# Kernel optimization log

Measured on AMD Instinct MI355X. Metric: run time of the kernel, lower is better.

The kernel has to match this reference:

```python
import jax, jax.numpy as jnp
import numpy as np

N_NODES = 100000
N_EDGES = 600000
IN_CH = 64
HID = 256


def setup_inputs() -> dict:
    key = jax.random.key(0)
    ks = jax.random.split(key, 8)
    x = jax.random.normal(ks[0], (N_NODES, IN_CH), dtype=jnp.float32)
    edge_index = jax.random.randint(ks[1], (2, N_EDGES), 0, N_NODES, dtype=jnp.int64)
    # Glorot-ish init for weights, zero bias (matches PyG GCNConv defaults)
    W1 = jax.random.normal(ks[2], (IN_CH, HID), dtype=jnp.float32) * (1.0 / np.sqrt(IN_CH))
    b1 = jnp.zeros((HID,), dtype=jnp.float32)
    W2 = jax.random.normal(ks[3], (HID, HID), dtype=jnp.float32) * (1.0 / np.sqrt(HID))
    b2 = jnp.zeros((HID,), dtype=jnp.float32)
    W3 = jax.random.normal(ks[4], (HID, HID), dtype=jnp.float32) * (1.0 / np.sqrt(HID))
    b3 = jnp.zeros((HID,), dtype=jnp.float32)
    return {"x": x, "edge_index": edge_index, "W1": W1, "b1": b1,
            "W2": W2, "b2": b2, "W3": W3, "b3": b3}


def _gcn_conv(x, src, dst, norm, W, b):
    # PyG GCNConv (add_self_loops=False): h = x W; out_i = sum_{j->i} norm_ij h_j; out += b
    h = x @ W                                   # [N, d_out]
    msg = h[src] * norm[:, None]                # [E, d_out] gather + scale
    out = jax.ops.segment_sum(msg, dst, num_segments=x.shape[0])
    return out + b


def reference(x, edge_index, W1, b1, W2, b2, W3, b3):
    src, dst = edge_index[0], edge_index[1]
    # symmetric degree normalization (gcn_norm without self loops)
    deg = jax.ops.segment_sum(jnp.ones_like(dst, dtype=x.dtype), dst,
                              num_segments=x.shape[0])
    dinv = jnp.where(deg > 0, jax.lax.rsqrt(jnp.maximum(deg, 1.0)), 0.0)
    norm = dinv[src] * dinv[dst]                # [E]

    h = jax.nn.elu(_gcn_conv(x, src, dst, norm, W1, b1))
    h = jax.nn.elu(_gcn_conv(h, src, dst, norm, W2, b2))
    h = jax.nn.elu(_gcn_conv(h, src, dst, norm, W3, b3))
    return h
```

## Files before the change

### kernel.cpp

```cpp
#include <hip/hip_runtime.h>
#include <hip/hip_bf16.h>
#include <math.h>


#define THREADS 256

typedef __attribute__((ext_vector_type(8))) short short8;
typedef __attribute__((ext_vector_type(4))) float f32x4;

__global__ void k_deg(const int* __restrict__ dst, int* __restrict__ deg, int E) {
    int e = blockIdx.x * THREADS + threadIdx.x;
    if (e < E) atomicAdd(&deg[dst[e]], 1);
}

__global__ void k_dinv(const int* __restrict__ deg, float* __restrict__ dinv, int N) {
    int i = blockIdx.x * THREADS + threadIdx.x;
    if (i < N) {
        int d = deg[i];
        dinv[i] = (d > 0) ? rsqrtf((float)d) : 0.0f;
    }
}

__global__ void k_scan1(const int* __restrict__ deg, int* __restrict__ rowp,
                        int* __restrict__ bsums, int N) {
    __shared__ int s[THREADS];
    int idx = blockIdx.x * THREADS + threadIdx.x;
    int v = (idx < N) ? deg[idx] : 0;
    s[threadIdx.x] = v;
    __syncthreads();
    for (int off = 1; off < THREADS; off <<= 1) {
        int t = (threadIdx.x >= off) ? s[threadIdx.x - off] : 0;
        __syncthreads();
        s[threadIdx.x] += t;
        __syncthreads();
    }
    if (idx < N) rowp[idx] = s[threadIdx.x] - v;
    if (threadIdx.x == THREADS - 1) bsums[blockIdx.x] = s[threadIdx.x];
}

__global__ void k_scan2(int* __restrict__ bsums, int NB) {
    __shared__ int s[512];
    int v = (threadIdx.x < (unsigned)NB) ? bsums[threadIdx.x] : 0;
    s[threadIdx.x] = v;
    __syncthreads();
    for (int off = 1; off < 512; off <<= 1) {
        int t = (threadIdx.x >= (unsigned)off) ? s[threadIdx.x - off] : 0;
        __syncthreads();
        s[threadIdx.x] += t;
        __syncthreads();
    }
    if (threadIdx.x < (unsigned)NB) bsums[threadIdx.x] = s[threadIdx.x] - v;
}

__global__ void k_scan3(int* __restrict__ rowp, const int* __restrict__ bsums, int N) {
    int idx = blockIdx.x * THREADS + threadIdx.x;
    if (idx < N) rowp[idx] += bsums[blockIdx.x];
}

__global__ void k_fill(const int* __restrict__ src, const int* __restrict__ dst,
                       const float* __restrict__ dinv, const int* __restrict__ rowp,
                       int* __restrict__ cnt, int* __restrict__ esrc,
                       float* __restrict__ enorm, int E) {
    int e = blockIdx.x * THREADS + threadIdx.x;
    if (e >= E) return;
    int s = src[e], d = dst[e];
    int pos = rowp[d] + atomicAdd(&cnt[d], 1);
    esrc[pos]  = s;
    enorm[pos] = dinv[s] * dinv[d];
}

__device__ __forceinline__ unsigned bf16rn(float x) {
    unsigned u = __float_as_uint(x);
    return (u + 0x7FFFu + ((u >> 16) & 1u)) >> 16;
}
__device__ __forceinline__ void split1(float x, short8& h, short8& l, int e) {
    unsigned hb = bf16rn(x);
    float hf = __uint_as_float(hb << 16);
    h[e] = (short)hb;
    l[e] = (short)bf16rn(x - hf);
}
__device__ __forceinline__ void split4(float4 v, short8& h, short8& l, int e0) {
    split1(v.x, h, l, e0 + 0);
    split1(v.y, h, l, e0 + 1);
    split1(v.z, h, l, e0 + 2);
    split1(v.w, h, l, e0 + 3);
}

__global__ void k_wsplit2(const float* __restrict__ W, short* __restrict__ Bp, int K) {
    int idx = blockIdx.x * THREADS + threadIdx.x;
    if (idx >= K * 256) return;
    int k = idx >> 8;
    int c = idx & 255;
    int t = k >> 5, kb = (k >> 3) & 3, e = k & 7;
    int ct = c >> 4, r = c & 15;
    float w = W[(size_t)k * 256 + c];
    unsigned hb = bf16rn(w);
    float hf = __uint_as_float(hb << 16);
    size_t base = ((size_t)(t * 16 + ct) * 2) * 512 + (kb * 16 + r) * 8 + e;
    Bp[base]       = (short)hb;
    Bp[base + 512] = (short)bf16rn(w - hf);
}

__device__ __forceinline__ void load_lds16(const void* g, void* l) {
    __builtin_amdgcn_global_load_lds(
        (const __attribute__((address_space(1))) void*)g,
        (__attribute__((address_space(3))) void*)l, 16, 0, 0);
}

template <int K>
__global__ __launch_bounds__(256) void k_mgemm(const float* __restrict__ act,
                                               const short* __restrict__ Bpack,
                                               float* __restrict__ C, int N) {
    constexpr int NT = K / 32;
    __shared__ short Blds[2 * 16384];

    const int tid  = threadIdx.x;
    const int lane = tid & 63;
    const int wv   = tid >> 6;
    const int r    = lane & 15;
    const int kb   = lane >> 4;
    const int row0 = blockIdx.x * 128 + wv * 32;

    int ra = row0 + r;       if (ra >= N) ra = N - 1;
    int rb = row0 + 16 + r;  if (rb >= N) rb = N - 1;
    const float* apa = act + (size_t)ra * K + kb * 8;
    const float* apb = act + (size_t)rb * K + kb * 8;

    f32x4 acc0[16], acc1[16];
#pragma unroll
    for (int ct = 0; ct < 16; ++ct) { acc0[ct] = (f32x4)0.0f; acc1[ct] = (f32x4)0.0f; }

#pragma unroll
    for (int it = 0; it < 8; ++it)
        load_lds16(Bpack + it * 2048 + wv * 512 + lane * 8,
                   Blds + it * 2048 + wv * 512);
    float4 c00 = *(const float4*)(apa);
    float4 c01 = *(const float4*)(apa + 4);
    float4 c10 = *(const float4*)(apb);
    float4 c11 = *(const float4*)(apb + 4);
    __syncthreads();

    int cur = 0;
#pragma unroll 1
    for (int t = 0; t < NT; ++t) {
        float4 n00, n01, n10, n11;
        if (t + 1 < NT) {
            const short* src = Bpack + (size_t)(t + 1) * 16384;
            short* dst = Blds + (cur ^ 1) * 16384;
#pragma unroll
            for (int it = 0; it < 8; ++it)
                load_lds16(src + it * 2048 + wv * 512 + lane * 8,
                           dst + it * 2048 + wv * 512);
            n00 = *(const float4*)(apa + (t + 1) * 32);
            n01 = *(const float4*)(apa + (t + 1) * 32 + 4);
            n10 = *(const float4*)(apb + (t + 1) * 32);
            n11 = *(const float4*)(apb + (t + 1) * 32 + 4);
        }

        short8 ah0, al0, ah1, al1;
        split4(c00, ah0, al0, 0); split4(c01, ah0, al0, 4);
        split4(c10, ah1, al1, 0); split4(c11, ah1, al1, 4);

        const short* bb = Blds + cur * 16384;
#pragma unroll
        for (int ct = 0; ct < 16; ++ct) {
            short8 bh = *(const short8*)(bb + (ct * 2 + 0) * 512 + lane * 8);
            short8 bl = *(const short8*)(bb + (ct * 2 + 1) * 512 + lane * 8);
            acc0[ct] = __builtin_amdgcn_mfma_f32_16x16x32_bf16(ah0, bh, acc0[ct], 0, 0, 0);
            acc0[ct] = __builtin_amdgcn_mfma_f32_16x16x32_bf16(ah0, bl, acc0[ct], 0, 0, 0);
            acc0[ct] = __builtin_amdgcn_mfma_f32_16x16x32_bf16(al0, bh, acc0[ct], 0, 0, 0);
            acc1[ct] = __builtin_amdgcn_mfma_f32_16x16x32_bf16(ah1, bh, acc1[ct], 0, 0, 0);
            acc1[ct] = __builtin_amdgcn_mfma_f32_16x16x32_bf16(ah1, bl, acc1[ct], 0, 0, 0);
            acc1[ct] = __builtin_amdgcn_mfma_f32_16x16x32_bf16(al1, bh, acc1[ct], 0, 0, 0);
        }
        __syncthreads();

        if (t + 1 < NT) { c00 = n00; c01 = n01; c10 = n10; c11 = n11; }
        cur ^= 1;
    }

#pragma unroll
    for (int jr = 0; jr < 4; ++jr) {
        int g0 = row0 + kb * 4 + jr;
        if (g0 < N) {
            float* cp = C + (size_t)g0 * 256 + r;
#pragma unroll
            for (int ct = 0; ct < 16; ++ct) cp[ct * 16] = acc0[ct][jr];
        }
        int g1 = row0 + 16 + kb * 4 + jr;
        if (g1 < N) {
            float* cp = C + (size_t)g1 * 256 + r;
#pragma unroll
            for (int ct = 0; ct < 16; ++ct) cp[ct * 16] = acc1[ct][jr];
        }
    }
}

__device__ __forceinline__ float elu1(float x) {
    return x > 0.0f ? x : expm1f(x);
}

__global__ __launch_bounds__(256) void k_agg(const float* __restrict__ h,
                                             const int* __restrict__ rowp,
                                             const int* __restrict__ deg,
                                             const int* __restrict__ esrc,
                                             const float* __restrict__ enorm,
                                             const float* __restrict__ bias,
                                             float* __restrict__ out, int N) {
    int wave = threadIdx.x >> 6;
    int lane = threadIdx.x & 63;
    int node = blockIdx.x * 4 + wave;
    if (node >= N) return;

    int start = rowp[node];
    int cnt   = deg[node];

    float4 acc = make_float4(0.f, 0.f, 0.f, 0.f);
    float4 acc2 = make_float4(0.f, 0.f, 0.f, 0.f);
    int e = 0;
    for (; e + 2 <= cnt; e += 2) {
        int   s0 = esrc[start + e];
        int   s1 = esrc[start + e + 1];
        float n0 = enorm[start + e];
        float n1 = enorm[start + e + 1];
        float4 h0 = *(const float4*)&h[(size_t)s0 * 256 + lane * 4];
        float4 h1 = *(const float4*)&h[(size_t)s1 * 256 + lane * 4];
        acc.x += n0 * h0.x;  acc.y += n0 * h0.y;
        acc.z += n0 * h0.z;  acc.w += n0 * h0.w;
        acc2.x += n1 * h1.x; acc2.y += n1 * h1.y;
        acc2.z += n1 * h1.z; acc2.w += n1 * h1.w;
    }
    if (e < cnt) {
        int   s0 = esrc[start + e];
        float n0 = enorm[start + e];
        float4 h0 = *(const float4*)&h[(size_t)s0 * 256 + lane * 4];
        acc.x += n0 * h0.x; acc.y += n0 * h0.y;
        acc.z += n0 * h0.z; acc.w += n0 * h0.w;
    }
    acc.x += acc2.x; acc.y += acc2.y; acc.z += acc2.z; acc.w += acc2.w;

    float4 b4 = *(const float4*)&bias[lane * 4];
    float4 o;
    o.x = elu1(acc.x + b4.x);
    o.y = elu1(acc.y + b4.y);
    o.z = elu1(acc.z + b4.z);
    o.w = elu1(acc.w + b4.w);
    *(float4*)&out[(size_t)node * 256 + lane * 4] = o;
}

static inline size_t alignup(size_t x) { return (x + 255) & ~(size_t)255; }

extern "C" void kernel_launch(void* const* d_in, const int* in_sizes, int n_in,
                              void* d_out, int out_size, void* d_ws, size_t ws_size,
                              hipStream_t stream) {
    const float* x  = (const float*)d_in[0];
    const int*   ei = (const int*)d_in[1];
    const float* W1 = (const float*)d_in[2];
    const float* b1 = (const float*)d_in[3];
    const float* W2 = (const float*)d_in[4];
    const float* b2 = (const float*)d_in[5];
    const float* W3 = (const float*)d_in[6];
    const float* b3 = (const float*)d_in[7];
    float* out = (float*)d_out;

    const int N = in_sizes[0] / 64;
    const int E = in_sizes[1] / 2;
    const int* src = ei;
    const int* dst = ei + E;

    char* p = (char*)d_ws;
    int*   deg   = (int*)p;   p += alignup((size_t)N * 4);
    float* dinv  = (float*)p; p += alignup((size_t)N * 4);
    int*   rowp  = (int*)p;   p += alignup((size_t)N * 4);
    int*   cnt   = (int*)p;   p += alignup((size_t)N * 4);
    int*   esrc  = (int*)p;   p += alignup((size_t)E * 4);
    float* enorm = (float*)p; p += alignup((size_t)E * 4);
    const int NB = (N + THREADS - 1) / THREADS;
    int*   bsums = (int*)p;   p += alignup((size_t)NB * 4);
    short* Bpack = (short*)p; p += alignup((size_t)256 * 256 * 2 * 2);
    float* bufA  = (float*)p; p += alignup((size_t)N * 256 * 4);

    const int EB = (E + THREADS - 1) / THREADS;
    const int GB = (N + 127) / 128;
    const int AB = (N + 3) / 4;

    hipMemsetAsync(deg, 0, (size_t)N * 4, stream);
    hipMemsetAsync(cnt, 0, (size_t)N * 4, stream);

    k_deg<<<EB, THREADS, 0, stream>>>(dst, deg, E);
    k_dinv<<<NB, THREADS, 0, stream>>>(deg, dinv, N);
    k_scan1<<<NB, THREADS, 0, stream>>>(deg, rowp, bsums, N);
    k_scan2<<<1, 512, 0, stream>>>(bsums, NB);
    k_scan3<<<NB, THREADS, 0, stream>>>(rowp, bsums, N);
    k_fill<<<EB, THREADS, 0, stream>>>(src, dst, dinv, rowp, cnt, esrc, enorm, E);

    k_wsplit2<<<(64 * 256 + THREADS - 1) / THREADS, THREADS, 0, stream>>>(W1, Bpack, 64);
    k_mgemm<64><<<GB, THREADS, 0, stream>>>(x, Bpack, bufA, N);
    k_agg<<<AB, THREADS, 0, stream>>>(bufA, rowp, deg, esrc, enorm, b1, out, N);
    k_wsplit2<<<(256 * 256 + THREADS - 1) / THREADS, THREADS, 0, stream>>>(W2, Bpack, 256);
    k_mgemm<256><<<GB, THREADS, 0, stream>>>(out, Bpack, bufA, N);
    k_agg<<<AB, THREADS, 0, stream>>>(bufA, rowp, deg, esrc, enorm, b2, out, N);
    k_wsplit2<<<(256 * 256 + THREADS - 1) / THREADS, THREADS, 0, stream>>>(W3, Bpack, 256);
    k_mgemm<256><<<GB, THREADS, 0, stream>>>(out, Bpack, bufA, N);
    k_agg<<<AB, THREADS, 0, stream>>>(bufA, rowp, deg, esrc, enorm, b3, out, N);
}
```

Before: 650.8 us.

## Aggregate before GEMM and fuse bias plus ELU into GEMM epilogue

Reorders each GCN layer to aggregate neighbor features first (A·X) and then multiply by W, using linearity. The first layer now gathers 64-wide input rows instead of 256-wide projected rows, which cuts gather traffic for that layer. Bias and ELU move into the GEMM epilogue, removing the separate elementwise pass inside aggregation. The two memsets are merged into one by placing the buffers next to each other. Summation order changes, so floating-point rounding differs slightly from the reference.

```diff
diff --git a/kernel.cpp b/kernel.cpp
--- a/kernel.cpp
+++ b/kernel.cpp
@@ -107,9 +107,14 @@
         (__attribute__((address_space(3))) void*)l, 16, 0, 0);
 }
 
+__device__ __forceinline__ float elu1(float x) {
+    return x > 0.0f ? x : expm1f(x);
+}
+
 template <int K>
 __global__ __launch_bounds__(256) void k_mgemm(const float* __restrict__ act,
                                                const short* __restrict__ Bpack,
+                                               const float* __restrict__ bias,
                                                float* __restrict__ C, int N) {
     constexpr int NT = K / 32;
     __shared__ short Blds[2 * 16384];
@@ -179,34 +184,33 @@
         cur ^= 1;
     }
 
+    float bv[16];
+#pragma unroll
+    for (int ct = 0; ct < 16; ++ct) bv[ct] = bias[ct * 16 + r];
+
 #pragma unroll
     for (int jr = 0; jr < 4; ++jr) {
         int g0 = row0 + kb * 4 + jr;
         if (g0 < N) {
             float* cp = C + (size_t)g0 * 256 + r;
 #pragma unroll
-            for (int ct = 0; ct < 16; ++ct) cp[ct * 16] = acc0[ct][jr];
+            for (int ct = 0; ct < 16; ++ct) cp[ct * 16] = elu1(acc0[ct][jr] + bv[ct]);
         }
         int g1 = row0 + 16 + kb * 4 + jr;
         if (g1 < N) {
             float* cp = C + (size_t)g1 * 256 + r;
 #pragma unroll
-            for (int ct = 0; ct < 16; ++ct) cp[ct * 16] = acc1[ct][jr];
+            for (int ct = 0; ct < 16; ++ct) cp[ct * 16] = elu1(acc1[ct][jr] + bv[ct]);
         }
     }
 }
 
-__device__ __forceinline__ float elu1(float x) {
-    return x > 0.0f ? x : expm1f(x);
-}
-
-__global__ __launch_bounds__(256) void k_agg(const float* __restrict__ h,
-                                             const int* __restrict__ rowp,
-                                             const int* __restrict__ deg,
-                                             const int* __restrict__ esrc,
-                                             const float* __restrict__ enorm,
-                                             const float* __restrict__ bias,
-                                             float* __restrict__ out, int N) {
+__global__ __launch_bounds__(256) void k_aggp(const float* __restrict__ h,
+                                              const int* __restrict__ rowp,
+                                              const int* __restrict__ deg,
+                                              const int* __restrict__ esrc,
+                                              const float* __restrict__ enorm,
+                                              float* __restrict__ g, int N) {
     int wave = threadIdx.x >> 6;
     int lane = threadIdx.x & 63;
     int node = blockIdx.x * 4 + wave;
@@ -237,15 +241,41 @@
         acc.x += n0 * h0.x; acc.y += n0 * h0.y;
         acc.z += n0 * h0.z; acc.w += n0 * h0.w;
     }
-    acc.x += acc2.x; acc.y += acc2.y; acc.z += acc2.z; acc.w += acc2.w;
-
-    float4 b4 = *(const float4*)&bias[lane * 4];
     float4 o;
-    o.x = elu1(acc.x + b4.x);
-    o.y = elu1(acc.y + b4.y);
-    o.z = elu1(acc.z + b4.z);
-    o.w = elu1(acc.w + b4.w);
-    *(float4*)&out[(size_t)node * 256 + lane * 4] = o;
+    o.x = acc.x + acc2.x; o.y = acc.y + acc2.y;
+    o.z = acc.z + acc2.z; o.w = acc.w + acc2.w;
+    *(float4*)&g[(size_t)node * 256 + lane * 4] = o;
+}
+
+__global__ __launch_bounds__(256) void k_agg64(const float* __restrict__ x,
+                                               const int* __restrict__ rowp,
+                                               const int* __restrict__ deg,
+                                               const int* __restrict__ esrc,
+                                               const float* __restrict__ enorm,
+                                               float* __restrict__ g, int N) {
+    int wave = threadIdx.x >> 6;
+    int lane = threadIdx.x & 63;
+    int node = blockIdx.x * 4 + wave;
+    if (node >= N) return;
+
+    int start = rowp[node];
+    int cnt   = deg[node];
+
+    float a0 = 0.f, a1 = 0.f;
+    int e = 0;
+    for (; e + 2 <= cnt; e += 2) {
+        int   s0 = esrc[start + e];
+        int   s1 = esrc[start + e + 1];
+        float n0 = enorm[start + e];
+        float n1 = enorm[start + e + 1];
+        a0 += n0 * x[(size_t)s0 * 64 + lane];
+        a1 += n1 * x[(size_t)s1 * 64 + lane];
+    }
+    if (e < cnt) {
+        int s0 = esrc[start + e];
+        a0 += enorm[start + e] * x[(size_t)s0 * 64 + lane];
+    }
+    g[(size_t)node * 64 + lane] = a0 + a1;
 }
 
 static inline size_t alignup(size_t x) { return (x + 255) & ~(size_t)255; }
@@ -270,22 +300,21 @@
 
     char* p = (char*)d_ws;
     int*   deg   = (int*)p;   p += alignup((size_t)N * 4);
+    int*   cnt   = (int*)p;   p += alignup((size_t)N * 4);
     float* dinv  = (float*)p; p += alignup((size_t)N * 4);
     int*   rowp  = (int*)p;   p += alignup((size_t)N * 4);
-    int*   cnt   = (int*)p;   p += alignup((size_t)N * 4);
     int*   esrc  = (int*)p;   p += alignup((size_t)E * 4);
     float* enorm = (float*)p; p += alignup((size_t)E * 4);
     const int NB = (N + THREADS - 1) / THREADS;
     int*   bsums = (int*)p;   p += alignup((size_t)NB * 4);
     short* Bpack = (short*)p; p += alignup((size_t)256 * 256 * 2 * 2);
-    float* bufA  = (float*)p; p += alignup((size_t)N * 256 * 4);
+    float* G     = (float*)p; p += alignup((size_t)N * 256 * 4);
 
     const int EB = (E + THREADS - 1) / THREADS;
     const int GB = (N + 127) / 128;
     const int AB = (N + 3) / 4;
 
-    hipMemsetAsync(deg, 0, (size_t)N * 4, stream);
-    hipMemsetAsync(cnt, 0, (size_t)N * 4, stream);
+    hipMemsetAsync(deg, 0, alignup((size_t)N * 4) + (size_t)N * 4, stream);
 
     k_deg<<<EB, THREADS, 0, stream>>>(dst, deg, E);
     k_dinv<<<NB, THREADS, 0, stream>>>(deg, dinv, N);
@@ -294,13 +323,15 @@
     k_scan3<<<NB, THREADS, 0, stream>>>(rowp, bsums, N);
     k_fill<<<EB, THREADS, 0, stream>>>(src, dst, dinv, rowp, cnt, esrc, enorm, E);
 
+    k_agg64<<<AB, THREADS, 0, stream>>>(x, rowp, deg, esrc, enorm, G, N);
     k_wsplit2<<<(64 * 256 + THREADS - 1) / THREADS, THREADS, 0, stream>>>(W1, Bpack, 64);
-    k_mgemm<64><<<GB, THREADS, 0, stream>>>(x, Bpack, bufA, N);
-    k_agg<<<AB, THREADS, 0, stream>>>(bufA, rowp, deg, esrc, enorm, b1, out, N);
+    k_mgemm<64><<<GB, THREADS, 0, stream>>>(G, Bpack, b1, out, N);
+
+    k_aggp<<<AB, THREADS, 0, stream>>>(out, rowp, deg, esrc, enorm, G, N);
     k_wsplit2<<<(256 * 256 + THREADS - 1) / THREADS, THREADS, 0, stream>>>(W2, Bpack, 256);
-    k_mgemm<256><<<GB, THREADS, 0, stream>>>(out, Bpack, bufA, N);
-    k_agg<<<AB, THREADS, 0, stream>>>(bufA, rowp, deg, esrc, enorm, b2, out, N);
+    k_mgemm<256><<<GB, THREADS, 0, stream>>>(G, Bpack, b2, out, N);
+
+    k_aggp<<<AB, THREADS, 0, stream>>>(out, rowp, deg, esrc, enorm, G, N);
     k_wsplit2<<<(256 * 256 + THREADS - 1) / THREADS, THREADS, 0, stream>>>(W3, Bpack, 256);
-    k_mgemm<256><<<GB, THREADS, 0, stream>>>(out, Bpack, bufA, N);
-    k_agg<<<AB, THREADS, 0, stream>>>(bufA, rowp, deg, esrc, enorm, b3, out, N);
-}
+    k_mgemm<256><<<GB, THREADS, 0, stream>>>(G, Bpack, b3, out, N);
+}
```

After: 718.4 us. 1.1x slower.
